# Kernel tuning notes

Measured on AMD Instinct MI355X. Metric: run time of the kernel, lower is better.

Reference implementation:

```python
import jax, jax.numpy as jnp
import numpy as np

HIDDEN = 768
MLP = 4 * HIDDEN

def layernorm(x, g, b, eps=1e-5):
    mu = jnp.mean(x, axis=-1, keepdims=True)
    var = jnp.var(x, axis=-1, keepdims=True)
    return (x - mu) * jax.lax.rsqrt(var + eps) * g + b

def setup_inputs() -> dict:
    key = jax.random.key(0)
    ks = jax.random.split(key, 10)
    b, l, h = 8, 1024, HIDDEN
    s = 1.0 / np.sqrt(h)
    inp = {
        "x": jax.random.normal(ks[0], (b, l, h), dtype=jnp.float32),
        "Wq": jax.random.normal(ks[1], (h, h), dtype=jnp.float32) * s,
        "Wk": jax.random.normal(ks[2], (h, h), dtype=jnp.float32) * s,
        "Wv": jax.random.normal(ks[3], (h, h), dtype=jnp.float32) * s,
        "Wo": jax.random.normal(ks[4], (h, h), dtype=jnp.float32) * s,
        "W1": jax.random.normal(ks[5], (h, MLP), dtype=jnp.float32) * s,
        "b1": jnp.zeros((MLP,), dtype=jnp.float32),
        "W2": jax.random.normal(ks[6], (MLP, h), dtype=jnp.float32) * (1.0 / np.sqrt(MLP)),
        "b2": jnp.zeros((h,), dtype=jnp.float32),
        "g1": jnp.ones((h,), dtype=jnp.float32),
        "be1": jnp.zeros((h,), dtype=jnp.float32),
        "g2": jnp.ones((h,), dtype=jnp.float32),
        "be2": jnp.zeros((h,), dtype=jnp.float32),
        "n_heads": 12,
    }
    return inp

def reference(x, Wq, Wk, Wv, Wo, W1, b1, W2, b2, g1, be1, g2, be2, n_heads):
    b, l, h = x.shape
    d = h // n_heads
    # NOTE: faithful to source — heads are the LAST axis of a plain reshape,
    # and the second einsum contracts with K (not V), reproducing the original code.
    q = (x @ Wq).reshape(b, l, d, n_heads)
    k = (x @ Wk).reshape(b, l, d, n_heads)
    v = (x @ Wv).reshape(b, l, d, n_heads)  # computed but unused downstream, as in source
    scores = jnp.einsum('bldn,bmdn->blmn', q, k) / (d ** 0.5)
    attn = jax.nn.softmax(scores, axis=2)  # softmax over m (dim=2), as in source
    ctx = jnp.einsum('blmn,bmdn->bldn', attn, k).reshape(b, l, h)
    attn_out = ctx @ Wo
    x = x + attn_out
    x = layernorm(x, g1, be1)
    ff = (jax.nn.gelu(x @ W1 + b1, approximate=False) @ W2) + b2
    x = x + ff
    x = layernorm(x, g2, be2)
    return x
```

## Files before the change

kernel.cpp:

```cpp
#include <hip/hip_runtime.h>
#include <math.h>

typedef unsigned short u16;
typedef unsigned int u32;
typedef short bf16x8 __attribute__((ext_vector_type(8)));
typedef float f32x4 __attribute__((ext_vector_type(4)));

#define MFMA(a, b, c) __builtin_amdgcn_mfma_f32_16x16x32_bf16((a), (b), (c), 0, 0, 0)

#define GLOAD_LDS16(g, l)                                                              \
    __builtin_amdgcn_global_load_lds((const __attribute__((address_space(1))) void*)(g), \
                                     (__attribute__((address_space(3))) void*)(l), 16, 0, 0)

__device__ __forceinline__ u16 f2bf(float f) {
    u32 u = __float_as_uint(f);
    u32 r = (u + 0x7fffu + ((u >> 16) & 1u)) >> 16;
    return (u16)r;
}

__device__ __forceinline__ u16 f2bf_trunc(float f) {
    return (u16)(__float_as_uint(f) >> 16);
}

__device__ __forceinline__ float fast_gelu(float z) {
    float u = fminf(1.5957691216f * z * (1.0f + 0.044715f * z * z), 80.0f);
    float e = __expf(u);
    float r = __builtin_amdgcn_rcpf(e + 1.0f);
    return z * e * r;
}

__device__ void dev_xcast(const float* __restrict__ in, u16* __restrict__ out, int blk) {
    size_t i = ((size_t)blk * 256 + threadIdx.x) * 8;
    const float4* p = reinterpret_cast<const float4*>(in + i);
    float4 a = p[0], b = p[1];
    union { u16 u[8]; uint4 v; } o;
    o.u[0] = f2bf(a.x); o.u[1] = f2bf(a.y); o.u[2] = f2bf(a.z); o.u[3] = f2bf(a.w);
    o.u[4] = f2bf(b.x); o.u[5] = f2bf(b.y); o.u[6] = f2bf(b.z); o.u[7] = f2bf(b.w);
    *reinterpret_cast<uint4*>(out + i) = o.v;
}

__device__ void dev_transpose(const float* __restrict__ in, u16* __restrict__ out,
                              int K, int N, int bx, int by, float* tile ) {
    int k0 = by * 64, n0 = bx * 64;
    int t = threadIdx.x;
    for (int p = 0; p < 16; p++) {
        int idx = t + p * 256;
        int r = idx >> 6, c = idx & 63;
        tile[r * 65 + c] = in[(size_t)(k0 + r) * N + n0 + c];
    }
    __syncthreads();
    for (int p = 0; p < 16; p++) {
        int idx = t + p * 256;
        int nr = idx >> 6, nc = idx & 63;
        out[(size_t)(n0 + nr) * K + k0 + nc] = f2bf(tile[nc * 65 + nr]);
    }
}

__device__ void dev_wo(const float* __restrict__ in, u16* __restrict__ out,
                       int bx, int by, float* tile ) {
    int k0 = by * 96, n0 = bx * 64;
    int t = threadIdx.x;
    for (int p = 0; p < 24; p++) {
        int idx = t + p * 256;
        int r = idx >> 6, c = idx & 63;
        tile[r * 65 + c] = in[(size_t)(k0 + r) * 768 + n0 + c];
    }
    __syncthreads();
    for (int p = 0; p < 3; p++) {
        int idx = t + p * 256;
        int c = idx / 12, n = idx % 12;
        union { u16 u[8]; uint4 v; } o;
        for (int j = 0; j < 8; j++) o.u[j] = f2bf(tile[(j * 12 + n) * 65 + c]);
        *reinterpret_cast<uint4*>(&out[(size_t)(n0 + c) * 768 + n * 64 + by * 8]) = o.v;
    }
}

__global__ __launch_bounds__(256) void prep_k(const float* __restrict__ x,
                                              const float* __restrict__ Wq,
                                              const float* __restrict__ Wk,
                                              const float* __restrict__ Wo,
                                              const float* __restrict__ W1,
                                              const float* __restrict__ W2,
                                              u16* __restrict__ XB,
                                              u16* __restrict__ WQKT,
                                              u16* __restrict__ WOT,
                                              u16* __restrict__ W1T,
                                              u16* __restrict__ W2T) {
    __shared__ float tile[96 * 65];
    int bid = blockIdx.x;
    if (bid < 3072) {
        dev_xcast(x, XB, bid);
    } else if (bid < 3216) {
        int b = bid - 3072; dev_transpose(Wq, WQKT, 768, 768, b % 12, b / 12, tile);
    } else if (bid < 3360) {
        int b = bid - 3216; dev_transpose(Wk, WQKT + (size_t)768 * 768, 768, 768, b % 12, b / 12, tile);
    } else if (bid < 3456) {
        int b = bid - 3360; dev_wo(Wo, WOT, b % 12, b / 12, tile);
    } else if (bid < 4032) {
        int b = bid - 3456; dev_transpose(W1, W1T, 768, 3072, b % 48, b / 48, tile);
    } else {
        int b = bid - 4032; dev_transpose(W2, W2T, 3072, 768, b % 12, b / 12, tile);
    }
}

__global__ __launch_bounds__(256) void head_pack_k(const u16* __restrict__ in, int ld,
                                                   u16* __restrict__ out,
                                                   u16* __restrict__ outT) {
    __shared__ u16 tile[16 * 768];
    int b = blockIdx.y;
    int l0 = blockIdx.x * 16;
    int t = threadIdx.x;
    for (int p = 0; p < 6; p++) {
        int c = t + p * 256;
        int li = c / 96, dc = c % 96;
        *reinterpret_cast<uint4*>(&tile[li * 768 + dc * 8]) =
            *reinterpret_cast<const uint4*>(&in[(size_t)(b * 1024 + l0 + li) * ld + dc * 8]);
    }
    __syncthreads();
    for (int p = 0; p < 6; p++) {
        int c = t + p * 256;
        int n = c >> 7, rem = c & 127, li = rem >> 3, k8 = rem & 7;
        union { u16 u[8]; uint4 v; } o;
        for (int j = 0; j < 8; j++) o.u[j] = tile[li * 768 + (k8 * 8 + j) * 12 + n];
        *reinterpret_cast<uint4*>(&out[(size_t)((b * 12 + n) * 1024 + l0 + li) * 64 + k8 * 8]) = o.v;
    }
    for (int p = 0; p < 6; p++) {
        int c = t + p * 256;
        int n = c >> 7;
        int rem = c & 127;
        int d = rem >> 1;
        int half = rem & 1;
        union { u16 u[8]; uint4 v; } o;
        for (int j = 0; j < 8; j++) o.u[j] = tile[(half * 8 + j) * 768 + d * 12 + n];
        *reinterpret_cast<uint4*>(
            &outT[((size_t)(b * 12 + n) * 64 + d) * 1024 + l0 + half * 8]) = o.v;
    }
}

template <int EPI, int TM, bool AH = false>
__global__ __launch_bounds__(256) void gemm_bt_k(const u16* __restrict__ A,
                                                 const u16* __restrict__ BT,
                                                 int M, int N, int K, int NBX,
                                                 float* __restrict__ outF,
                                                 u16* __restrict__ outB,
                                                 const float* __restrict__ resid,
                                                 const float* __restrict__ bias) {
    constexpr int MI = TM / 32;
    constexpr int NS = (TM == 64) ? 4 : 3;
    __shared__ __align__(16) u16 As[NS][TM * 32];
    __shared__ __align__(16) u16 Bs[NS][128 * 32];

    int L = blockIdx.x;
    int bx = (L >> 3) % NBX;
    int by = (L / (8 * NBX)) * 8 + (L & 7);
    int m0 = by * TM, n0 = bx * 128;

    int t = threadIdx.x;
    int wave = t >> 6, lane = t & 63;
    int wr = (wave >> 1) * (TM / 2), wc = (wave & 1) * 64;
    int ln = lane & 15, quad = lane >> 4;
    int sw = quad ^ ((ln >> 1) & 3);

    int e0 = t, e1 = t + 256;
    int r0 = e0 >> 2, c0 = (e0 & 3) ^ ((r0 >> 1) & 3);
    int r1 = e1 >> 2, c1 = (e1 & 3) ^ ((r1 >> 1) & 3);
    const u16* A0 = A + (size_t)(m0 + r0) * K + c0 * 8;
    const u16* A1 = A + (size_t)(m0 + r1) * K + c1 * 8;
    const u16* B0 = BT + (size_t)(n0 + r0) * K + c0 * 8;
    const u16* B1 = BT + (size_t)(n0 + r1) * K + c1 * 8;
    const u16* Abase = nullptr;
    if constexpr (AH) {
        int m = m0 + r0;
        Abase = A + ((size_t)(m >> 10) * 12288 + (m & 1023)) * 64;
    }

    int nk = K >> 5;

    f32x4 acc[MI][4];
    for (int i = 0; i < MI; i++)
        for (int j = 0; j < 4; j++)
            for (int r = 0; r < 4; r++) acc[i][j][r] = 0.0f;

    for (int s = 0; s < NS - 1; s++) {
        if constexpr (AH) {
            int col8 = s * 4 + c0;
            GLOAD_LDS16(Abase + (col8 >> 3) * 65536 + (col8 & 7) * 8, &As[s][e0 * 8]);
        } else {
            GLOAD_LDS16(A0 + s * 32, &As[s][e0 * 8]);
            if constexpr (TM == 128) GLOAD_LDS16(A1 + s * 32, &As[s][e1 * 8]);
        }
        GLOAD_LDS16(B0 + s * 32, &Bs[s][e0 * 8]);
        GLOAD_LDS16(B1 + s * 32, &Bs[s][e1 * 8]);
    }

    for (int kb = 0; kb < nk; kb += NS) {
#pragma unroll
        for (int s = 0; s < NS; s++) {
            int k = kb + s;
            if constexpr (TM == 64) asm volatile("s_waitcnt vmcnt(6)" ::: "memory");
            else                    asm volatile("s_waitcnt vmcnt(4)" ::: "memory");
            asm volatile("s_barrier" ::: "memory");
            {
                int ks = k + NS - 1 < nk ? k + NS - 1 : nk - 1;
                int stage = (s + NS - 1) % NS;
                if constexpr (AH) {
                    int col8 = ks * 4 + c0;
                    GLOAD_LDS16(Abase + (col8 >> 3) * 65536 + (col8 & 7) * 8, &As[stage][e0 * 8]);
                } else {
                    GLOAD_LDS16(A0 + ks * 32, &As[stage][e0 * 8]);
                    if constexpr (TM == 128) GLOAD_LDS16(A1 + ks * 32, &As[stage][e1 * 8]);
                }
                GLOAD_LDS16(B0 + ks * 32, &Bs[stage][e0 * 8]);
                GLOAD_LDS16(B1 + ks * 32, &Bs[stage][e1 * 8]);
            }
            const u16* as = As[s];
            const u16* bs = Bs[s];
            bf16x8 afr[MI], bfr[4];
            for (int i = 0; i < MI; i++)
                afr[i] = *reinterpret_cast<const bf16x8*>(&as[(wr + i * 16 + ln) * 32 + sw * 8]);
            for (int j = 0; j < 4; j++)
                bfr[j] = *reinterpret_cast<const bf16x8*>(&bs[(wc + j * 16 + ln) * 32 + sw * 8]);
            for (int i = 0; i < MI; i++)
                for (int j = 0; j < 4; j++)
                    acc[i][j] = MFMA(afr[i], bfr[j], acc[i][j]);
        }
    }

    for (int i = 0; i < MI; i++) {
        for (int j = 0; j < 4; j++) {
            int col = n0 + wc + j * 16 + ln;
            for (int r = 0; r < 4; r++) {
                int row = m0 + wr + i * 16 + quad * 4 + r;
                size_t idx = (size_t)row * N + col;
                float v = acc[i][j][r];
                if constexpr (EPI == 1) {
                    outF[idx] = resid[idx] + v;
                } else if constexpr (EPI == 2) {
                    outB[idx] = f2bf(fast_gelu(v + bias[col]));
                } else if constexpr (EPI == 3) {
                    outF[idx] = resid[idx] + v + bias[col];
                } else {
                    outB[idx] = f2bf(col < 768 ? v * 0.18033688011112042f : v);
                }
            }
        }
    }
}

__global__ __launch_bounds__(256) void attention_k(const u16* __restrict__ QB, int ldq,
                                                   const u16* __restrict__ KH,
                                                   const u16* __restrict__ KHT,
                                                   u16* __restrict__ CTXH) {
    __shared__ __align__(16) u16 Ks[64 * 72];
    __shared__ __align__(16) u16 KsT[64 * 72];
    __shared__ __align__(16) u16 Pl[4][16 * 72];
    int bh = blockIdx.y;
    int b = bh / 12, n = bh % 12;
    int l0 = blockIdx.x * 64;
    int t = threadIdx.x, wave = t >> 6, lane = t & 63;
    int ln = lane & 15, quad = lane >> 4;
    int lw = l0 + wave * 16;

    bf16x8 a0, a1;
    {
        union { u16 u[8]; bf16x8 v; } q0, q1;
        const u16* qrow = QB + (size_t)(b * 1024 + lw + ln) * ldq + n;
        for (int j = 0; j < 8; j++) {
            q0.u[j] = qrow[(quad * 8 + j) * 12];
            q1.u[j] = qrow[(32 + quad * 8 + j) * 12];
        }
        a0 = q0.v; a1 = q1.v;
    }

    f32x4 o[4];
    for (int dt = 0; dt < 4; dt++)
        for (int r = 0; r < 4; r++) o[dt][r] = 0.0f;
    float lst[4];
    for (int r = 0; r < 4; r++) lst[r] = 0.0f;

    const u16* Kbase  = KH  + (size_t)bh * 65536;
    const u16* KTbase = KHT + (size_t)bh * 65536;
    int mi = t & 63, ds = (t >> 6) * 16;

    uint4 kva = *reinterpret_cast<const uint4*>(&Kbase[(size_t)mi * 64 + ds]);
    uint4 kvb = *reinterpret_cast<const uint4*>(&Kbase[(size_t)mi * 64 + ds + 8]);
    uint4 kta = *reinterpret_cast<const uint4*>(&KTbase[(size_t)mi * 1024 + ds]);
    uint4 ktb = *reinterpret_cast<const uint4*>(&KTbase[(size_t)mi * 1024 + ds + 8]);

    for (int mb = 0; mb < 16; mb++) {
        __syncthreads();
        *reinterpret_cast<uint4*>(&Ks[mi * 72 + ds]) = kva;
        *reinterpret_cast<uint4*>(&Ks[mi * 72 + ds + 8]) = kvb;
        *reinterpret_cast<uint4*>(&KsT[mi * 72 + ds]) = kta;
        *reinterpret_cast<uint4*>(&KsT[mi * 72 + ds + 8]) = ktb;
        __syncthreads();

        {
            int mnext = (mb + 1 < 16 ? mb + 1 : 15) * 64;
            kva = *reinterpret_cast<const uint4*>(&Kbase[(size_t)(mnext + mi) * 64 + ds]);
            kvb = *reinterpret_cast<const uint4*>(&Kbase[(size_t)(mnext + mi) * 64 + ds + 8]);
            kta = *reinterpret_cast<const uint4*>(&KTbase[(size_t)mi * 1024 + mnext + ds]);
            ktb = *reinterpret_cast<const uint4*>(&KTbase[(size_t)mi * 1024 + mnext + ds + 8]);
        }

        f32x4 st[4];
        for (int nt = 0; nt < 4; nt++) {
            bf16x8 bk0 = *reinterpret_cast<bf16x8*>(&Ks[(nt * 16 + ln) * 72 + quad * 8]);
            bf16x8 bk1 = *reinterpret_cast<bf16x8*>(&Ks[(nt * 16 + ln) * 72 + 32 + quad * 8]);
            f32x4 z;
            for (int r = 0; r < 4; r++) z[r] = 0.0f;
            z = MFMA(a0, bk0, z);
            st[nt] = MFMA(a1, bk1, z);
        }

        for (int r = 0; r < 4; r++) {
            int row = quad * 4 + r;
            float psum = 0.0f;
            for (int nt = 0; nt < 4; nt++) {
                float p = exp2f(st[nt][r]);
                psum += p;
                Pl[wave][row * 72 + nt * 16 + ln] = f2bf_trunc(p);
            }
            lst[r] += psum;
        }

        bf16x8 pf0 = *reinterpret_cast<bf16x8*>(&Pl[wave][ln * 72 + quad * 8]);
        bf16x8 pf1 = *reinterpret_cast<bf16x8*>(&Pl[wave][ln * 72 + 32 + quad * 8]);
        for (int dt = 0; dt < 4; dt++) {
            bf16x8 bk0 = *reinterpret_cast<bf16x8*>(&KsT[(dt * 16 + ln) * 72 + quad * 8]);
            bf16x8 bk1 = *reinterpret_cast<bf16x8*>(&KsT[(dt * 16 + ln) * 72 + 32 + quad * 8]);
            o[dt] = MFMA(pf0, bk0, o[dt]);
            o[dt] = MFMA(pf1, bk1, o[dt]);
        }
    }

    for (int r = 0; r < 4; r++)
        for (int off = 1; off < 16; off <<= 1) lst[r] += __shfl_xor(lst[r], off, 64);

    u16* out = CTXH + (size_t)bh * 65536;
    for (int r = 0; r < 4; r++) {
        float inv = 1.0f / lst[r];
        int row = lw + quad * 4 + r;
        for (int dt = 0; dt < 4; dt++)
            out[(size_t)row * 64 + dt * 16 + ln] = f2bf(o[dt][r] * inv);
    }
}

__global__ __launch_bounds__(256) void layernorm_k(const float* __restrict__ in,
                                                   float* __restrict__ outF,
                                                   u16* __restrict__ outB,
                                                   const float* __restrict__ g,
                                                   const float* __restrict__ be) {
    __shared__ float red[8];
    int row = blockIdx.x;
    int t = threadIdx.x;
    const float* p = in + (size_t)row * 768;
    float v0 = p[t], v1 = p[t + 256], v2 = p[t + 512];
    float s = v0 + v1 + v2;
    float ss = v0 * v0 + v1 * v1 + v2 * v2;
    for (int off = 32; off >= 1; off >>= 1) {
        s += __shfl_xor(s, off, 64);
        ss += __shfl_xor(ss, off, 64);
    }
    int wave = t >> 6, lane = t & 63;
    if (lane == 0) { red[wave] = s; red[4 + wave] = ss; }
    __syncthreads();
    float S = red[0] + red[1] + red[2] + red[3];
    float SS = red[4] + red[5] + red[6] + red[7];
    float mean = S * (1.0f / 768.0f);
    float var = SS * (1.0f / 768.0f) - mean * mean;
    float rstd = rsqrtf(var + 1e-5f);
    float o0 = (v0 - mean) * rstd * g[t] + be[t];
    float o1 = (v1 - mean) * rstd * g[t + 256] + be[t + 256];
    float o2 = (v2 - mean) * rstd * g[t + 512] + be[t + 512];
    float* q = outF + (size_t)row * 768;
    q[t] = o0; q[t + 256] = o1; q[t + 512] = o2;
    if (outB) {
        u16* qb = outB + (size_t)row * 768;
        qb[t] = f2bf(o0); qb[t + 256] = f2bf(o1); qb[t + 512] = f2bf(o2);
    }
}

extern "C" void kernel_launch(void* const* d_in, const int* in_sizes, int n_in,
                              void* d_out, int out_size, void* d_ws, size_t ws_size,
                              hipStream_t stream) {
    const float* x   = (const float*)d_in[0];
    const float* Wq  = (const float*)d_in[1];
    const float* Wk  = (const float*)d_in[2];
    const float* Wo  = (const float*)d_in[4];
    const float* W1  = (const float*)d_in[5];
    const float* b1  = (const float*)d_in[6];
    const float* W2  = (const float*)d_in[7];
    const float* b2  = (const float*)d_in[8];
    const float* g1  = (const float*)d_in[9];
    const float* be1 = (const float*)d_in[10];
    const float* g2  = (const float*)d_in[11];
    const float* be2 = (const float*)d_in[12];
    float* out = (float*)d_out;

    const int S = 8192, H = 768, MLP4 = 3072, H2 = 1536;

    char* ws = (char*)d_ws;
    u16* XB   = (u16*)ws;  ws += (size_t)S * H * 2;
    u16* WQKT = (u16*)ws;  ws += (size_t)H2 * H * 2;
    u16* WOT  = (u16*)ws;  ws += (size_t)H * H * 2;
    u16* W1T  = (u16*)ws;  ws += (size_t)H * MLP4 * 2;
    u16* W2T  = (u16*)ws;  ws += (size_t)H * MLP4 * 2;
    u16* QKB  = (u16*)ws;  ws += (size_t)S * H2 * 2;
    u16* KH   = (u16*)ws;  ws += (size_t)S * H * 2;
    float* Y  = (float*)ws; ws += (size_t)S * H * 4;
    u16* HB   = (u16*)ws;  ws += (size_t)S * MLP4 * 2;

    u16* CTXH = XB;
    u16* X1B  = QKB;
    u16* KHT  = HB;

    prep_k<<<4608, 256, 0, stream>>>(x, Wq, Wk, Wo, W1, W2, XB, WQKT, WOT, W1T, W2T);

    gemm_bt_k<4, 128><<<12 * 64, 256, 0, stream>>>(XB, WQKT, S, H2, H, 12, nullptr, QKB, nullptr, nullptr);

    head_pack_k<<<dim3(64, 8), 256, 0, stream>>>(QKB + H, H2, KH, KHT);
    attention_k<<<dim3(16, 96), 256, 0, stream>>>(QKB, H2, KH, KHT, CTXH);

    gemm_bt_k<1, 64, true><<<6 * 128, 256, 0, stream>>>(CTXH, WOT, S, H, H, 6, Y, nullptr, x, nullptr);
    layernorm_k<<<S, 256, 0, stream>>>(Y, Y, X1B, g1, be1);

    gemm_bt_k<2, 128><<<24 * 64, 256, 0, stream>>>(X1B, W1T, S, MLP4, H, 24, nullptr, HB, nullptr, b1);
    gemm_bt_k<3, 64><<<6 * 128, 256, 0, stream>>>(HB, W2T, S, H, MLP4, 6, Y, nullptr, Y, b2);
    layernorm_k<<<S, 256, 0, stream>>>(Y, out, nullptr, g2, be2);
}
```

Before: 396.4 us.

## Split K across two block halves for Wo and W2 GEMMs, sum in layernorm

```diff
diff --git a/kernel.cpp b/kernel.cpp
--- a/kernel.cpp
+++ b/kernel.cpp
@@ -137,7 +137,7 @@
     }
 }
 
-template <int EPI, int TM, bool AH = false>
+template <int EPI, int TM, bool AH = false, int NSO = 0, bool KSPLIT = false>
 __global__ __launch_bounds__(256) void gemm_bt_k(const u16* __restrict__ A,
                                                  const u16* __restrict__ BT,
                                                  int M, int N, int K, int NBX,
@@ -146,11 +146,18 @@
                                                  const float* __restrict__ resid,
                                                  const float* __restrict__ bias) {
     constexpr int MI = TM / 32;
-    constexpr int NS = (TM == 64) ? 4 : 3;
+    constexpr int NS = NSO ? NSO : ((TM == 64) ? 4 : 3);
+    constexpr int LPS = (TM == 128) ? 4 : 3;
+    constexpr int VC = LPS * (NS - 2);
     __shared__ __align__(16) u16 As[NS][TM * 32];
     __shared__ __align__(16) u16 Bs[NS][128 * 32];
 
     int L = blockIdx.x;
+    int kp = 0;
+    if constexpr (KSPLIT) {
+        int half = gridDim.x >> 1;
+        if (L >= half) { kp = 1; L -= half; }
+    }
     int bx = (L >> 3) % NBX;
     int by = (L / (8 * NBX)) * 8 + (L & 7);
     int m0 = by * TM, n0 = bx * 128;
@@ -164,10 +171,14 @@
     int e0 = t, e1 = t + 256;
     int r0 = e0 >> 2, c0 = (e0 & 3) ^ ((r0 >> 1) & 3);
     int r1 = e1 >> 2, c1 = (e1 & 3) ^ ((r1 >> 1) & 3);
-    const u16* A0 = A + (size_t)(m0 + r0) * K + c0 * 8;
-    const u16* A1 = A + (size_t)(m0 + r1) * K + c1 * 8;
-    const u16* B0 = BT + (size_t)(n0 + r0) * K + c0 * 8;
-    const u16* B1 = BT + (size_t)(n0 + r1) * K + c1 * 8;
+    int kofs = 0;
+    if constexpr (KSPLIT) kofs = kp * (K >> 1);
+    int ahk = 0;
+    if constexpr (KSPLIT && AH) ahk = kp * (K >> 4);
+    const u16* A0 = A + (size_t)(m0 + r0) * K + kofs + c0 * 8;
+    const u16* A1 = A + (size_t)(m0 + r1) * K + kofs + c1 * 8;
+    const u16* B0 = BT + (size_t)(n0 + r0) * K + kofs + c0 * 8;
+    const u16* B1 = BT + (size_t)(n0 + r1) * K + kofs + c1 * 8;
     const u16* Abase = nullptr;
     if constexpr (AH) {
         int m = m0 + r0;
@@ -175,6 +186,7 @@
     }
 
     int nk = K >> 5;
+    if constexpr (KSPLIT) nk >>= 1;
 
     f32x4 acc[MI][4];
     for (int i = 0; i < MI; i++)
@@ -183,7 +195,7 @@
 
     for (int s = 0; s < NS - 1; s++) {
         if constexpr (AH) {
-            int col8 = s * 4 + c0;
+            int col8 = ahk + s * 4 + c0;
             GLOAD_LDS16(Abase + (col8 >> 3) * 65536 + (col8 & 7) * 8, &As[s][e0 * 8]);
         } else {
             GLOAD_LDS16(A0 + s * 32, &As[s][e0 * 8]);
@@ -197,14 +209,16 @@
 #pragma unroll
         for (int s = 0; s < NS; s++) {
             int k = kb + s;
-            if constexpr (TM == 64) asm volatile("s_waitcnt vmcnt(6)" ::: "memory");
-            else                    asm volatile("s_waitcnt vmcnt(4)" ::: "memory");
+            if constexpr (VC == 6)      asm volatile("s_waitcnt vmcnt(6)" ::: "memory");
+            else if constexpr (VC == 4) asm volatile("s_waitcnt vmcnt(4)" ::: "memory");
+            else if constexpr (VC == 3) asm volatile("s_waitcnt vmcnt(3)" ::: "memory");
+            else                        asm volatile("s_waitcnt vmcnt(0)" ::: "memory");
             asm volatile("s_barrier" ::: "memory");
             {
                 int ks = k + NS - 1 < nk ? k + NS - 1 : nk - 1;
                 int stage = (s + NS - 1) % NS;
                 if constexpr (AH) {
-                    int col8 = ks * 4 + c0;
+                    int col8 = ahk + ks * 4 + c0;
                     GLOAD_LDS16(Abase + (col8 >> 3) * 65536 + (col8 & 7) * 8, &As[stage][e0 * 8]);
                 } else {
                     GLOAD_LDS16(A0 + ks * 32, &As[stage][e0 * 8]);
@@ -234,11 +248,21 @@
                 size_t idx = (size_t)row * N + col;
                 float v = acc[i][j][r];
                 if constexpr (EPI == 1) {
-                    outF[idx] = resid[idx] + v;
+                    if constexpr (KSPLIT) {
+                        if (kp == 0) outF[idx] = resid[idx] + v;
+                        else reinterpret_cast<float*>(outB)[idx] = v;
+                    } else {
+                        outF[idx] = resid[idx] + v;
+                    }
                 } else if constexpr (EPI == 2) {
                     outB[idx] = f2bf(fast_gelu(v + bias[col]));
                 } else if constexpr (EPI == 3) {
-                    outF[idx] = resid[idx] + v + bias[col];
+                    if constexpr (KSPLIT) {
+                        if (kp == 0) outF[idx] = resid[idx] + v + bias[col];
+                        else reinterpret_cast<float*>(outB)[idx] = v;
+                    } else {
+                        outF[idx] = resid[idx] + v + bias[col];
+                    }
                 } else {
                     outB[idx] = f2bf(col < 768 ? v * 0.18033688011112042f : v);
                 }
@@ -350,12 +374,17 @@
                                                    float* __restrict__ outF,
                                                    u16* __restrict__ outB,
                                                    const float* __restrict__ g,
-                                                   const float* __restrict__ be) {
+                                                   const float* __restrict__ be,
+                                                   const float* __restrict__ in2) {
     __shared__ float red[8];
     int row = blockIdx.x;
     int t = threadIdx.x;
     const float* p = in + (size_t)row * 768;
     float v0 = p[t], v1 = p[t + 256], v2 = p[t + 512];
+    if (in2) {
+        const float* p2 = in2 + (size_t)row * 768;
+        v0 += p2[t]; v1 += p2[t + 256]; v2 += p2[t + 512];
+    }
     float s = v0 + v1 + v2;
     float ss = v0 * v0 + v1 * v1 + v2 * v2;
     for (int off = 32; off >= 1; off >>= 1) {
@@ -414,6 +443,8 @@
     u16* CTXH = XB;
     u16* X1B  = QKB;
     u16* KHT  = HB;
+    float* WoP = (float*)HB;
+    float* Y1 = (float*)QKB;
 
     prep_k<<<4608, 256, 0, stream>>>(x, Wq, Wk, Wo, W1, W2, XB, WQKT, WOT, W1T, W2T);
 
@@ -422,10 +453,10 @@
     head_pack_k<<<dim3(64, 8), 256, 0, stream>>>(QKB + H, H2, KH, KHT);
     attention_k<<<dim3(16, 96), 256, 0, stream>>>(QKB, H2, KH, KHT, CTXH);
 
-    gemm_bt_k<1, 64, true><<<6 * 128, 256, 0, stream>>>(CTXH, WOT, S, H, H, 6, Y, nullptr, x, nullptr);
-    layernorm_k<<<S, 256, 0, stream>>>(Y, Y, X1B, g1, be1);
+    gemm_bt_k<1, 64, true, 3, true><<<2 * 6 * 128, 256, 0, stream>>>(CTXH, WOT, S, H, H, 6, Y, (u16*)WoP, x, nullptr);
+    layernorm_k<<<S, 256, 0, stream>>>(Y, Y, X1B, g1, be1, WoP);
 
     gemm_bt_k<2, 128><<<24 * 64, 256, 0, stream>>>(X1B, W1T, S, MLP4, H, 24, nullptr, HB, nullptr, b1);
-    gemm_bt_k<3, 64><<<6 * 128, 256, 0, stream>>>(HB, W2T, S, H, MLP4, 6, Y, nullptr, Y, b2);
-    layernorm_k<<<S, 256, 0, stream>>>(Y, out, nullptr, g2, be2);
-}
+    gemm_bt_k<3, 64, false, 3, true><<<2 * 6 * 128, 256, 0, stream>>>(HB, W2T, S, H, MLP4, 6, Y, (u16*)Y1, Y, b2);
+    layernorm_k<<<S, 256, 0, stream>>>(Y, out, nullptr, g2, be2, Y1);
+}
```

Result: slower. 419.0 us (+5.7%).
